# Optimization experiments

Measured on AMD Instinct MI355X. Metric: run time of the kernel, lower is better.

Reference implementation:

```python
import jax, jax.numpy as jnp
import numpy as np

N_NODES = 50000
N_REL = 4
N_EDGE = 160000
H = 128
OUT = 100
L_HID = 2
N_QUERY = 8192


def setup_inputs() -> dict:
    key = jax.random.key(0)
    ks = jax.random.split(key, 10)
    s = 1.0 / np.sqrt(H)
    return {
        "feature": jax.random.normal(ks[0], (N_NODES, H), dtype=jnp.float32),
        "Wr_h": jax.random.normal(ks[1], (L_HID, N_REL, H, H), dtype=jnp.float32) * s,
        "Ws_h": jax.random.normal(ks[2], (L_HID, H, H), dtype=jnp.float32) * s,
        "Wr_o": jax.random.normal(ks[3], (N_REL, H, OUT), dtype=jnp.float32) * s,
        "Ws_o": jax.random.normal(ks[4], (H, OUT), dtype=jnp.float32) * s,
        "edge_src": jax.random.randint(ks[5], (N_REL, N_EDGE), 0, N_NODES, dtype=jnp.int64),
        "edge_dst": jax.random.randint(ks[6], (N_REL, N_EDGE), 0, N_NODES, dtype=jnp.int64),
        "head_idx": jax.random.randint(ks[7], (N_QUERY,), 0, N_NODES, dtype=jnp.int64),
        "tail_idx": jax.random.randint(ks[8], (N_QUERY,), 0, N_NODES, dtype=jnp.int64),
    }


def _rgcn_layer(h, edge_src, edge_dst, inv_deg, Wr, Ws, activate):
    # per-relation gather of source features: [R, E, H]
    msgs = h[edge_src]
    # per-relation scatter-add into destination nodes: [R, N, H]
    agg = jax.vmap(lambda m, d: jax.ops.segment_sum(m, d, num_segments=h.shape[0]))(msgs, edge_dst)
    agg = agg * inv_deg[..., None]  # mean (right) normalization per relation
    out = h @ Ws + jnp.einsum("rnh,rho->no", agg, Wr)
    return jax.nn.relu(out) if activate else out


def reference(feature, Wr_h, Ws_h, Wr_o, Ws_o, edge_src, edge_dst, head_idx, tail_idx):
    n = feature.shape[0]
    # per-relation in-degree, computed once (graph structure is fixed)
    deg = jax.vmap(lambda d: jax.ops.segment_sum(
        jnp.ones(d.shape, feature.dtype), d, num_segments=n))(edge_dst)  # [R, N]
    inv_deg = 1.0 / jnp.maximum(deg, 1.0)
    h = feature
    for l in range(Wr_h.shape[0]):
        h = _rgcn_layer(h, edge_src, edge_dst, inv_deg, Wr_h[l], Ws_h[l], activate=True)
    h = _rgcn_layer(h, edge_src, edge_dst, inv_deg, Wr_o, Ws_o, activate=False)
    heads = h[head_idx]  # [Q, OUT]
    tails = h[tail_idx]  # [Q, OUT]
    return (heads, tails)
```

## Files before the change

kernel.cpp:

```cpp
#include <hip/hip_runtime.h>
#include <hip/hip_bf16.h>

#define NN 50000
#define NR 4
#define NE 160000
#define HD 128
#define OD 100
#define NQ 8192
#define NB_SCAN 196

#define NB_COUNT 2500
#define NB_CONV  6250
#define NB_PREPW 960

typedef __attribute__((ext_vector_type(8))) short bf16x8;
typedef __attribute__((ext_vector_type(4))) float f32x4;
typedef __attribute__((ext_vector_type(4))) int int4v;

static __device__ __forceinline__ unsigned short f2bf(float f) {
    union { float f; unsigned int u; } v; v.f = f;
    unsigned int u = v.u;
    unsigned int r = u + 0x7FFFu + ((u >> 16) & 1u);
    return (unsigned short)(r >> 16);
}
static __device__ __forceinline__ float bflo(unsigned int v) {
    union { unsigned int u; float f; } x; x.u = v << 16; return x.f;
}
static __device__ __forceinline__ float bfhi(unsigned int v) {
    union { unsigned int u; float f; } x; x.u = v & 0xffff0000u; return x.f;
}


__global__ __launch_bounds__(256) void prep_merged_kernel(
        const int* __restrict__ edge_dst, int* __restrict__ deg,
        const float* __restrict__ feature, unsigned short* __restrict__ h,
        const float* __restrict__ Ws_h, const float* __restrict__ Wr_h,
        const float* __restrict__ Ws_o, const float* __restrict__ Wr_o,
        unsigned short* __restrict__ Wt) {
    const int b = blockIdx.x;
    if (b < NB_COUNT) {
        const int i = b * 256 + threadIdx.x;
        const int r = i / NE;
        atomicAdd(&deg[r * NN + edge_dst[i]], 1);
    } else if (b < NB_COUNT + NB_CONV) {
        const int i = ((b - NB_COUNT) * 256 + threadIdx.x) * 4;
        h[i + 0] = f2bf(feature[i + 0]);
        h[i + 1] = f2bf(feature[i + 1]);
        h[i + 2] = f2bf(feature[i + 2]);
        h[i + 3] = f2bf(feature[i + 3]);
    } else {
        const int idx = (b - NB_COUNT - NB_CONV) * 256 + threadIdx.x;
        const int l = idx / (128 * 640);
        const int rem = idx % (128 * 640);
        const int c = rem / 640;
        const int k = rem % 640;
        float v = 0.0f;
        if (l < 2) {
            if (k < HD) v = Ws_h[(l * HD + k) * HD + c];
            else {
                int r = (k - HD) >> 7, kk = (k - HD) & 127;
                v = Wr_h[((l * NR + r) * HD + kk) * HD + c];
            }
        } else if (c < OD) {
            if (k < HD) v = Ws_o[k * OD + c];
            else {
                int r = (k - HD) >> 7, kk = (k - HD) & 127;
                v = Wr_o[(r * HD + kk) * OD + c];
            }
        }
        Wt[idx] = f2bf(v);
    }
}


__global__ __launch_bounds__(256) void scanA_kernel(const int* __restrict__ deg,
                                                    int* __restrict__ excl,
                                                    int* __restrict__ bsum) {
    const int r = blockIdx.x / NB_SCAN;
    const int b = blockIdx.x % NB_SCAN;
    const int tid = threadIdx.x;
    const int idx = b * 256 + tid;
    int v = (idx < NN) ? deg[r * NN + idx] : 0;
    __shared__ int buf[256];
    buf[tid] = v; __syncthreads();
    int sum = v;
    for (int off = 1; off < 256; off <<= 1) {
        int t = (tid >= off) ? buf[tid - off] : 0;
        __syncthreads();
        sum += t; buf[tid] = sum;
        __syncthreads();
    }
    if (idx < NN) excl[r * NN + idx] = sum - v;
    if (tid == 255) bsum[r * NB_SCAN + b] = sum;
}

__global__ __launch_bounds__(256) void scanC_kernel(const int* __restrict__ excl,
                                                    const int* __restrict__ bsum,
                                                    int* __restrict__ row_start,
                                                    int* __restrict__ cursor) {
    const int r = blockIdx.x / NB_SCAN;
    const int b = blockIdx.x % NB_SCAN;
    const int tid = threadIdx.x;
    __shared__ int buf[256];
    buf[tid] = (tid < b) ? bsum[r * NB_SCAN + tid] : 0;
    __syncthreads();
    for (int off = 128; off > 0; off >>= 1) {
        if (tid < off) buf[tid] += buf[tid + off];
        __syncthreads();
    }
    const int prefix = buf[0];
    const int idx = b * 256 + tid;
    if (idx < NN) {
        int v = excl[r * NN + idx] + prefix;
        row_start[r * (NN + 1) + idx] = v;
        cursor[r * NN + idx] = v;
    }
    if (b == 0 && tid == 0) row_start[r * (NN + 1) + NN] = NE;
}

__global__ __launch_bounds__(256) void fill_csr_kernel(const int* __restrict__ edge_src,
                                                       const int* __restrict__ edge_dst,
                                                       int* __restrict__ cursor,
                                                       int* __restrict__ csr_src) {
    const int i = blockIdx.x * 256 + threadIdx.x;
    const int r = i / NE;
    const int dst = edge_dst[i];
    const int pos = atomicAdd(&cursor[r * NN + dst], 1);
    csr_src[r * NE + pos] = edge_src[i];
}


template<int MODE>
__global__ __launch_bounds__(512, 2)
void fused_kernel(const unsigned short* __restrict__ h,
                  const unsigned short* __restrict__ Bt,
                  const int* __restrict__ row_start,
                  const int* __restrict__ csr_src,
                  void* __restrict__ outp, int M) {
    __shared__ __align__(16) char lds[40960];
    const int tid = threadIdx.x;
    const int m0 = blockIdx.x * 32;
    const int lane = tid & 63;
    const int w = tid >> 6;

    {
        const int row = tid >> 4, kb = (tid & 15) * 16;
        int gr = m0 + row; if (gr >= M) gr = M - 1;
        int4v v = *(const int4v*)((const char*)h + (size_t)gr * 256 + kb);
        *(int4v*)(lds + row * 256 + (kb ^ ((row & 7) << 4))) = v;
    }

    {
        const int g = lane >> 4, li = lane & 15;
        const int* __restrict__ csr = csr_src + (size_t)g * NE;
        const char* hp = (const char*)h + li * 16;

#pragma unroll
        for (int i = 0; i < 4; ++i) {
            const int n = m0 + (w << 2) + i;
            const bool vn = n < M;
            const int s = vn ? row_start[g * (NN + 1) + n] : 0;
            const int e = vn ? row_start[g * (NN + 1) + n + 1] : 0;

            f32x4 a0 = {0.f, 0.f, 0.f, 0.f}, a1 = {0.f, 0.f, 0.f, 0.f};
            int t = s;
            int sC = 0;
            int4v v0 = {0,0,0,0}, v1 = {0,0,0,0};
            {
                int sA = 0, sB = 0;
                if (t     < e) sA = csr[t];
                if (t + 1 < e) sB = csr[t + 1];
                if (t + 2 < e) sC = csr[t + 2];
                if (t     < e) v0 = *(const int4v*)(hp + (size_t)sA * 256);
                if (t + 1 < e) v1 = *(const int4v*)(hp + (size_t)sB * 256);
            }
            while (__any(t < e)) {
                const bool act = t < e;
                const int4v vc = v0;
                v0 = v1;
                if (t + 2 < e) v1 = *(const int4v*)(hp + (size_t)sC * 256);
                sC = (t + 3 < e) ? csr[t + 3] : 0;
                if (act) {
                    const unsigned int* vu = (const unsigned int*)&vc;
                    a0[0] += bflo(vu[0]); a0[1] += bfhi(vu[0]);
                    a0[2] += bflo(vu[1]); a0[3] += bfhi(vu[1]);
                    a1[0] += bflo(vu[2]); a1[1] += bfhi(vu[2]);
                    a1[2] += bflo(vu[3]); a1[3] += bfhi(vu[3]);
                }
                ++t;
            }
            const float wd = 1.0f / fmaxf((float)(e - s), 1.0f);
            unsigned int p0 = (unsigned int)f2bf(wd * a0[0]) | ((unsigned int)f2bf(wd * a0[1]) << 16);
            unsigned int p1 = (unsigned int)f2bf(wd * a0[2]) | ((unsigned int)f2bf(wd * a0[3]) << 16);
            unsigned int p2 = (unsigned int)f2bf(wd * a1[0]) | ((unsigned int)f2bf(wd * a1[1]) << 16);
            unsigned int p3 = (unsigned int)f2bf(wd * a1[2]) | ((unsigned int)f2bf(wd * a1[3]) << 16);
            const int row = (w << 2) + i;
            const int cb = g * 256 + li * 16;
            *(int4v*)(lds + 8192 + row * 1024 + (cb ^ ((row & 7) << 4))) =
                (int4v){(int)p0, (int)p1, (int)p2, (int)p3};
        }
    }
    __syncthreads();

    const int lr = lane & 15;
    const int lg = lane >> 4;
    const char* bB = (const char*)Bt + (size_t)(w * 16 + lr) * 1280;

    f32x4 acc[2];
    acc[0] = (f32x4){0.f, 0.f, 0.f, 0.f};
    acc[1] = (f32x4){0.f, 0.f, 0.f, 0.f};

#pragma unroll
    for (int kb = 0; kb < 20; ++kb) {
        const int kByte = kb * 64 + lg * 16;
        bf16x8 bfr = *(const bf16x8*)(bB + kByte);
#pragma unroll
        for (int mi = 0; mi < 2; mi++) {
            const int row = mi * 16 + lr;
            int off;
            if (kb < 4) off = row * 256 + (kByte ^ ((row & 7) << 4));
            else        off = 8192 + row * 1024 + ((kByte - 256) ^ ((row & 7) << 4));
            bf16x8 af = *(const bf16x8*)(lds + off);
            acc[mi] = __builtin_amdgcn_mfma_f32_16x16x32_bf16(af, bfr, acc[mi], 0, 0, 0);
        }
    }

    __syncthreads();

    if (MODE == 0) {
#pragma unroll
        for (int mi = 0; mi < 2; mi++) {
            const int col = w * 16 + lr;
#pragma unroll
            for (int j = 0; j < 4; j++) {
                const int row = mi * 16 + lg * 4 + j;
                *(unsigned short*)(lds + row * 256 + col * 2) =
                    f2bf(fmaxf(acc[mi][j], 0.f));
            }
        }
        __syncthreads();
        unsigned short* o = (unsigned short*)outp;
        const int row = tid >> 4, kb = (tid & 15) * 16;
        const int grow = m0 + row;
        if (grow < M)
            *(int4v*)((char*)o + (size_t)grow * 256 + kb) = *(const int4v*)(lds + row * 256 + kb);
    } else {
#pragma unroll
        for (int mi = 0; mi < 2; mi++) {
            const int col = w * 16 + lr;
#pragma unroll
            for (int j = 0; j < 4; j++) {
                const int row = mi * 16 + lg * 4 + j;
                *(float*)(lds + row * 512 + col * 4) = acc[mi][j];
            }
        }
        __syncthreads();
        float* o = (float*)outp;
#pragma unroll
        for (int i = 0; i < 2; i++) {
            const int c = tid + i * 512;
            const int row = c >> 5, o16 = (c & 31) * 16;
            const int grow = m0 + row;
            if (grow < M)
                *(int4v*)((char*)o + (size_t)grow * 512 + o16) = *(const int4v*)(lds + row * 512 + o16);
        }
    }
}


__global__ __launch_bounds__(256) void gather_out_kernel(const float* __restrict__ hOut,
                                                         const int* __restrict__ head,
                                                         const int* __restrict__ tail,
                                                         float* __restrict__ out) {
    const int gid = blockIdx.x * 256 + threadIdx.x;
    const int q = gid >> 5, c = gid & 31;
    if (q >= 2 * NQ || c >= 25) return;
    const int node = (q < NQ) ? head[q] : tail[q - NQ];
    f32x4 v = *(const f32x4*)(hOut + (size_t)node * 128 + c * 4);
    *(f32x4*)(out + (size_t)q * OD + c * 4) = v;
}


extern "C" void kernel_launch(void* const* d_in, const int* in_sizes, int n_in,
                              void* d_out, int out_size, void* d_ws, size_t ws_size,
                              hipStream_t stream) {
    const float* feature = (const float*)d_in[0];
    const float* Wr_h    = (const float*)d_in[1];
    const float* Ws_h    = (const float*)d_in[2];
    const float* Wr_o    = (const float*)d_in[3];
    const float* Ws_o    = (const float*)d_in[4];
    const int* edge_src  = (const int*)d_in[5];
    const int* edge_dst  = (const int*)d_in[6];
    const int* head_idx  = (const int*)d_in[7];
    const int* tail_idx  = (const int*)d_in[8];
    float* out = (float*)d_out;

    char* ws = (char*)d_ws;
    size_t off = 0;
    auto alloc = [&](size_t bytes) -> void* {
        void* p = ws + off;
        off += (bytes + 255) & ~(size_t)255;
        return p;
    };
    unsigned short* hA   = (unsigned short*)alloc((size_t)NN * HD * 2);
    unsigned short* hB   = (unsigned short*)alloc((size_t)NN * HD * 2);
    float*          hOut = (float*)alloc((size_t)NN * 128 * 4);
    unsigned short* Wt   = (unsigned short*)alloc((size_t)3 * 128 * 640 * 2);
    int*            deg  = (int*)alloc((size_t)NR * NN * 4);
    int*            rowS = (int*)alloc((size_t)NR * (NN + 1) * 4);
    int*            curs = (int*)alloc((size_t)NR * NN * 4);
    int*            csrS = (int*)alloc((size_t)NR * NE * 4 + 64);
    int*            excl = (int*)alloc((size_t)NR * NN * 4);
    int*            bsum = (int*)alloc((size_t)NR * NB_SCAN * 4);
    (void)ws_size;

    hipMemsetAsync(deg, 0, (size_t)NR * NN * 4, stream);
    prep_merged_kernel<<<NB_COUNT + NB_CONV + NB_PREPW, 256, 0, stream>>>(
        edge_dst, deg, feature, hA, Ws_h, Wr_h, Ws_o, Wr_o, Wt);
    scanA_kernel<<<NR * NB_SCAN, 256, 0, stream>>>(deg, excl, bsum);
    scanC_kernel<<<NR * NB_SCAN, 256, 0, stream>>>(excl, bsum, rowS, curs);
    fill_csr_kernel<<<NB_COUNT, 256, 0, stream>>>(edge_src, edge_dst, curs, csrS);

    const int fblocks = (NN + 31) / 32;
    unsigned short* WtH0 = Wt;
    unsigned short* WtH1 = Wt + 128 * 640;
    unsigned short* WtO  = Wt + 2 * 128 * 640;

    fused_kernel<0><<<fblocks, 512, 0, stream>>>(hA, WtH0, rowS, csrS, hB, NN);
    fused_kernel<0><<<fblocks, 512, 0, stream>>>(hB, WtH1, rowS, csrS, hA, NN);
    fused_kernel<1><<<fblocks, 512, 0, stream>>>(hA, WtO,  rowS, csrS, hOut, NN);

    gather_out_kernel<<<(2 * NQ * 32 + 255) / 256, 256, 0, stream>>>(hOut, head_idx, tail_idx, out);
}
```

Baseline: 273.1 us.

## Batch first eight neighbor gathers per row and raise launch-bounds occupancy hint

The per-row CSR gather loop is restructured. The boundaries for four consecutive rows are loaded once, then up to eight source indices and their feature vectors are issued together before any accumulation, with a plain tail loop for rows that have more neighbors. This replaces the previous depth-two software-pipelined wave-synchronous loop and is meant to expose more memory-level parallelism for the short average degree (about 3.2). The launch bound minimum blocks is also raised from 2 to 8, which caps registers per thread and may cause spills given the eight int4 vectors held live.

```diff
diff --git a/kernel.cpp b/kernel.cpp
--- a/kernel.cpp
+++ b/kernel.cpp
@@ -131,7 +131,7 @@
 
 
 template<int MODE>
-__global__ __launch_bounds__(512, 2)
+__global__ __launch_bounds__(512, 8)
 void fused_kernel(const unsigned short* __restrict__ h,
                   const unsigned short* __restrict__ Bt,
                   const int* __restrict__ row_start,
@@ -154,46 +154,56 @@
         const int g = lane >> 4, li = lane & 15;
         const int* __restrict__ csr = csr_src + (size_t)g * NE;
         const char* hp = (const char*)h + li * 16;
-
-#pragma unroll
+        const int n0 = m0 + (w << 2);
+        const int rsB = g * (NN + 1);
+
+        int bnd[5];
+#pragma unroll
+        for (int i = 0; i < 5; i++) {
+            int n = n0 + i; if (n > M) n = M;
+            bnd[i] = row_start[rsB + n];
+        }
+
+#pragma unroll 1
         for (int i = 0; i < 4; ++i) {
-            const int n = m0 + (w << 2) + i;
-            const bool vn = n < M;
-            const int s = vn ? row_start[g * (NN + 1) + n] : 0;
-            const int e = vn ? row_start[g * (NN + 1) + n + 1] : 0;
+            const int s = bnd[i], e = bnd[i + 1];
+
+            int sj[8];
+#pragma unroll
+            for (int j = 0; j < 8; j++) sj[j] = (s + j < e) ? csr[s + j] : 0;
+
+            int4v vj[8];
+#pragma unroll
+            for (int j = 0; j < 8; j++) {
+                if (s + j < e) vj[j] = *(const int4v*)(hp + (size_t)sj[j] * 256);
+                else           vj[j] = (int4v){0, 0, 0, 0};
+            }
 
             f32x4 a0 = {0.f, 0.f, 0.f, 0.f}, a1 = {0.f, 0.f, 0.f, 0.f};
-            int t = s;
-            int sC = 0;
-            int4v v0 = {0,0,0,0}, v1 = {0,0,0,0};
-            {
-                int sA = 0, sB = 0;
-                if (t     < e) sA = csr[t];
-                if (t + 1 < e) sB = csr[t + 1];
-                if (t + 2 < e) sC = csr[t + 2];
-                if (t     < e) v0 = *(const int4v*)(hp + (size_t)sA * 256);
-                if (t + 1 < e) v1 = *(const int4v*)(hp + (size_t)sB * 256);
-            }
-            while (__any(t < e)) {
-                const bool act = t < e;
-                const int4v vc = v0;
-                v0 = v1;
-                if (t + 2 < e) v1 = *(const int4v*)(hp + (size_t)sC * 256);
-                sC = (t + 3 < e) ? csr[t + 3] : 0;
-                if (act) {
-                    const unsigned int* vu = (const unsigned int*)&vc;
-                    a0[0] += bflo(vu[0]); a0[1] += bfhi(vu[0]);
-                    a0[2] += bflo(vu[1]); a0[3] += bfhi(vu[1]);
-                    a1[0] += bflo(vu[2]); a1[1] += bfhi(vu[2]);
-                    a1[2] += bflo(vu[3]); a1[3] += bfhi(vu[3]);
-                }
-                ++t;
-            }
-            const float wd = 1.0f / fmaxf((float)(e - s), 1.0f);
-            unsigned int p0 = (unsigned int)f2bf(wd * a0[0]) | ((unsigned int)f2bf(wd * a0[1]) << 16);
-            unsigned int p1 = (unsigned int)f2bf(wd * a0[2]) | ((unsigned int)f2bf(wd * a0[3]) << 16);
-            unsigned int p2 = (unsigned int)f2bf(wd * a1[0]) | ((unsigned int)f2bf(wd * a1[1]) << 16);
-            unsigned int p3 = (unsigned int)f2bf(wd * a1[2]) | ((unsigned int)f2bf(wd * a1[3]) << 16);
+#pragma unroll
+            for (int j = 0; j < 8; j++) {
+                const unsigned int* vu = (const unsigned int*)&vj[j];
+                a0[0] += bflo(vu[0]); a0[1] += bfhi(vu[0]);
+                a0[2] += bflo(vu[1]); a0[3] += bfhi(vu[1]);
+                a1[0] += bflo(vu[2]); a1[1] += bfhi(vu[2]);
+                a1[2] += bflo(vu[3]); a1[3] += bfhi(vu[3]);
+            }
+
+            for (int t = s + 8; t < e; ++t) {
+                const int src = csr[t];
+                const int4v v = *(const int4v*)(hp + (size_t)src * 256);
+                const unsigned int* vu = (const unsigned int*)&v;
+                a0[0] += bflo(vu[0]); a0[1] += bfhi(vu[0]);
+                a0[2] += bflo(vu[1]); a0[3] += bfhi(vu[1]);
+                a1[0] += bflo(vu[2]); a1[1] += bfhi(vu[2]);
+                a1[2] += bflo(vu[3]); a1[3] += bfhi(vu[3]);
+            }
+
+            const float inv = 1.0f / fmaxf((float)(e - s), 1.0f);
+            unsigned int p0 = (unsigned int)f2bf(inv * a0[0]) | ((unsigned int)f2bf(inv * a0[1]) << 16);
+            unsigned int p1 = (unsigned int)f2bf(inv * a0[2]) | ((unsigned int)f2bf(inv * a0[3]) << 16);
+            unsigned int p2 = (unsigned int)f2bf(inv * a1[0]) | ((unsigned int)f2bf(inv * a1[1]) << 16);
+            unsigned int p3 = (unsigned int)f2bf(inv * a1[2]) | ((unsigned int)f2bf(inv * a1[3]) << 16);
             const int row = (w << 2) + i;
             const int cb = g * 256 + li * 16;
             *(int4v*)(lds + 8192 + row * 1024 + (cb ^ ((row & 7) << 4))) =
```

Result: faster. 259.9 us (-4.8%).
